# Kernel optimization log

Measured on AMD Instinct MI355X. Metric: run time of the kernel, lower is better.

The kernel has to match this reference:

```python
import jax, jax.numpy as jnp
import numpy as np

HIDDEN = 2048
INTER = 8192          # shared expert FFN
MOE_INTER = 1024      # routed expert FFN
N_ROUTED = 8
NUM_LOCAL = 8
TOP_K = 2
B, S = 4, 2048


def _mlp(x, gw, uw, dw):
    # down(swish(gate(x)) * up(x)); weights stored as (out, in) like nn.Linear
    g = x @ gw.T
    u = x @ uw.T
    return (g * jax.nn.sigmoid(g) * u) @ dw.T


def setup_inputs() -> dict:
    key = jax.random.key(0)
    ks = jax.random.split(key, 8)
    std = 0.02
    return {
        "hidden_states": jax.random.normal(ks[0], (B, S, HIDDEN), jnp.float32),
        "router_weight": jax.random.normal(ks[1], (N_ROUTED, HIDDEN), jnp.float32) * std,
        "sh_gate": jax.random.normal(ks[2], (INTER, HIDDEN), jnp.float32) * std,
        "sh_up": jax.random.normal(ks[3], (INTER, HIDDEN), jnp.float32) * std,
        "sh_down": jax.random.normal(ks[4], (HIDDEN, INTER), jnp.float32) * std,
        # NaiveMoe always uses experts[0]; only expert-0 weights participate.
        "r_gate": jax.random.normal(ks[5], (MOE_INTER, HIDDEN), jnp.float32) * std,
        "r_up": jax.random.normal(ks[6], (MOE_INTER, HIDDEN), jnp.float32) * std,
        "r_down": jax.random.normal(ks[7], (HIDDEN, MOE_INTER), jnp.float32) * std,
    }


def reference(hidden_states, router_weight, sh_gate, sh_up, sh_down, r_gate, r_up, r_down):
    Bsz, Seq, H = hidden_states.shape
    x = hidden_states.reshape(-1, H)                              # [T, H]

    # Router: float32 logits, top-k, softmax over the selected k
    logits = x.astype(jnp.float32) @ router_weight.astype(jnp.float32).T  # [T, E]
    topk_vals, topk_idx = jax.lax.top_k(logits, TOP_K)            # [T, K]
    topk_w = jax.nn.softmax(topk_vals, axis=-1)                   # [T, K]

    # Original dispatch loop applies experts[0] for every expert_id in
    # range(NUM_LOCAL); a token contributes its slot weight iff that slot's
    # routed index is < NUM_LOCAL. Net effect: per-token combined weight.
    slot_mask = (topk_idx < NUM_LOCAL).astype(topk_w.dtype)       # [T, K]
    comb_w = jnp.sum(topk_w * slot_mask, axis=-1).astype(x.dtype)  # [T]

    shared = _mlp(x, sh_gate, sh_up, sh_down)                     # [T, H]
    routed = _mlp(x, r_gate, r_up, r_down) * comb_w[:, None]      # [T, H]

    return (shared + routed).reshape(Bsz, Seq, H)
```

## Files before the change

### kernel.cpp

```cpp
#include <hip/hip_runtime.h>
#include <hip/hip_bf16.h>
#include <stdint.h>
#include <stddef.h>

#define HID   2048
#define INTER 8192
#define MOE_I 1024
#define TOK   8192

using bf16 = __hip_bfloat16;
typedef __attribute__((ext_vector_type(8))) short short8;
typedef __attribute__((ext_vector_type(4))) float f32x4;

__device__ __forceinline__ void gload_lds16(const bf16* g, bf16* l) {
    __builtin_amdgcn_global_load_lds(
        (const __attribute__((address_space(1))) void*)g,
        (__attribute__((address_space(3))) void*)l,
        16, 0, 0);
}

__device__ __forceinline__ short8 cvt8(float4 a, float4 b) {
    union { short8 s; bf16 h[8]; } u;
    u.h[0] = __float2bfloat16(a.x); u.h[1] = __float2bfloat16(a.y);
    u.h[2] = __float2bfloat16(a.z); u.h[3] = __float2bfloat16(a.w);
    u.h[4] = __float2bfloat16(b.x); u.h[5] = __float2bfloat16(b.y);
    u.h[6] = __float2bfloat16(b.z); u.h[7] = __float2bfloat16(b.w);
    return u.s;
}

__global__ void cast_f32_to_bf16(const float* __restrict__ in,
                                 bf16* __restrict__ out, int n4) {
    int stride = gridDim.x * blockDim.x;
    for (int i = blockIdx.x * blockDim.x + threadIdx.x; i < n4; i += stride) {
        float4 v = reinterpret_cast<const float4*>(in)[i];
        union { uint64_t u; bf16 h[4]; } o;
        o.h[0] = __float2bfloat16(v.x); o.h[1] = __float2bfloat16(v.y);
        o.h[2] = __float2bfloat16(v.z); o.h[3] = __float2bfloat16(v.w);
        reinterpret_cast<uint64_t*>(out)[i] = o.u;
    }
}


__global__ __launch_bounds__(512) void gemm8_gu(
    const bf16* __restrict__ X, const bf16* __restrict__ Wg,
    const bf16* __restrict__ Wu, bf16* __restrict__ H,
    int M, int N, int K)
{
    constexpr int STRM = 128 * 64;
    constexpr int SLOT = 3 * STRM;
    __shared__ __align__(16) bf16 lds[3 * SLOT];

    const int tid  = threadIdx.x;
    const int lane = tid & 63;
    const int wave = tid >> 6;
    const int n0 = blockIdx.x * 128;
    const int m0 = blockIdx.y * 128;

    const int srow = tid >> 3;
    const int scol = (((tid & 7) ^ (srow & 7)) << 3);
    const bf16* pA = X  + (size_t)(m0 + srow) * K + scol;
    const bf16* pG = Wg + (size_t)(n0 + srow) * K + scol;
    const bf16* pU = Wu + (size_t)(n0 + srow) * K + scol;
    const size_t rsk = (size_t)64 * K;
    bf16* dl = lds + tid * 8;

    const int wm = (wave >> 2) * 64;
    const int wn = (wave & 3) * 32;
    const int r16 = lane & 15;
    const int kq  = lane >> 4;
    const int cswz0 = ((kq       ^ (lane & 7)) << 4);
    const int cswz1 = (((4 + kq) ^ (lane & 7)) << 4);
    const char* lb = (const char*)lds;

    int roffA[4], roffW[2];
#pragma unroll
    for (int i = 0; i < 4; i++) roffA[i] = (wm + 16 * i + r16) * 128;
#pragma unroll
    for (int j = 0; j < 2; j++) roffW[j] = (wn + 16 * j + r16) * 128;

    f32x4 accg[4][2] = {};
    f32x4 accu[4][2] = {};
    const int NS = K >> 6;

#pragma unroll
    for (int s = 0; s < 2; s++) {
        bf16* d = dl + s * SLOT;
        const bf16* qa = pA + (size_t)s * 64;
        const bf16* qg = pG + (size_t)s * 64;
        const bf16* qu = pU + (size_t)s * 64;
        gload_lds16(qa,       d);
        gload_lds16(qg,       d + STRM);
        gload_lds16(qu,       d + 2 * STRM);
        gload_lds16(qa + rsk, d + 4096);
        gload_lds16(qg + rsk, d + STRM + 4096);
        gload_lds16(qu + rsk, d + 2 * STRM + 4096);
    }

    int cs = 0, ss = 2;
    for (int s = 0; s < NS; s++) {
        const int sp = (s + 2 < NS) ? (s + 2) : (NS - 1);
        const size_t ko = (size_t)sp * 64;
        const bf16* qa = pA + ko;
        const bf16* qg = pG + ko;
        const bf16* qu = pU + ko;
        bf16* d = dl + ss * SLOT;
        const char* cb = lb + (size_t)cs * (SLOT * 2);

        asm volatile("s_waitcnt vmcnt(6)" ::: "memory");
        __builtin_amdgcn_s_barrier();
        __builtin_amdgcn_sched_barrier(0);

        gload_lds16(qa, d);
        gload_lds16(qg, d + STRM);
        gload_lds16(qu, d + 2 * STRM);
        {
            short8 a[4], g[2], u[2];
#pragma unroll
            for (int i = 0; i < 4; i++)
                a[i] = *(const short8*)(cb + roffA[i] + cswz0);
#pragma unroll
            for (int j = 0; j < 2; j++) {
                g[j] = *(const short8*)(cb + (STRM * 2) + roffW[j] + cswz0);
                u[j] = *(const short8*)(cb + (STRM * 4) + roffW[j] + cswz0);
            }
            asm volatile("s_waitcnt lgkmcnt(0)" ::: "memory");
            __builtin_amdgcn_sched_barrier(0);
            __builtin_amdgcn_s_setprio(1);
#pragma unroll
            for (int i = 0; i < 4; i++)
#pragma unroll
                for (int j = 0; j < 2; j++) {
                    accg[i][j] = __builtin_amdgcn_mfma_f32_16x16x32_bf16(a[i], g[j], accg[i][j], 0, 0, 0);
                    accu[i][j] = __builtin_amdgcn_mfma_f32_16x16x32_bf16(a[i], u[j], accu[i][j], 0, 0, 0);
                }
            __builtin_amdgcn_s_setprio(0);
        }

        gload_lds16(qa + rsk, d + 4096);
        gload_lds16(qg + rsk, d + STRM + 4096);
        gload_lds16(qu + rsk, d + 2 * STRM + 4096);
        {
            short8 a[4], g[2], u[2];
#pragma unroll
            for (int i = 0; i < 4; i++)
                a[i] = *(const short8*)(cb + roffA[i] + cswz1);
#pragma unroll
            for (int j = 0; j < 2; j++) {
                g[j] = *(const short8*)(cb + (STRM * 2) + roffW[j] + cswz1);
                u[j] = *(const short8*)(cb + (STRM * 4) + roffW[j] + cswz1);
            }
            asm volatile("s_waitcnt lgkmcnt(0)" ::: "memory");
            __builtin_amdgcn_sched_barrier(0);
            __builtin_amdgcn_s_setprio(1);
#pragma unroll
            for (int i = 0; i < 4; i++)
#pragma unroll
                for (int j = 0; j < 2; j++) {
                    accg[i][j] = __builtin_amdgcn_mfma_f32_16x16x32_bf16(a[i], g[j], accg[i][j], 0, 0, 0);
                    accu[i][j] = __builtin_amdgcn_mfma_f32_16x16x32_bf16(a[i], u[j], accu[i][j], 0, 0, 0);
                }
            __builtin_amdgcn_s_setprio(0);
        }

        cs = (cs == 2) ? 0 : cs + 1;
        ss = (ss == 2) ? 0 : ss + 1;
    }
    asm volatile("s_waitcnt vmcnt(0)" ::: "memory");

#pragma unroll
    for (int i = 0; i < 4; i++) {
        const int rowb = m0 + wm + 16 * i + (lane >> 4) * 4;
#pragma unroll
        for (int j = 0; j < 2; j++) {
            const int col = n0 + wn + 16 * j + r16;
#pragma unroll
            for (int r = 0; r < 4; r++) {
                float g = accg[i][j][r];
                float u = accu[i][j][r];
                float h = g * u / (1.0f + __expf(-g));
                H[(size_t)(rowb + r) * N + col] = __float2bfloat16(h);
            }
        }
    }
}

__global__ __launch_bounds__(512) void gemm8_down(
    const bf16* __restrict__ Ha, const bf16* __restrict__ Bs,
    long ldBs, long col0,
    const bf16* __restrict__ Hb, const bf16* __restrict__ Br,
    long ldBr, float* __restrict__ OUT,
    int M, int N, int Ka, int Kb, int acc)
{
    constexpr int STRM = 128 * 64;
    constexpr int SLOT = 3 * STRM;
    __shared__ __align__(16) bf16 lds[3 * SLOT];

    const int tid  = threadIdx.x;
    const int lane = tid & 63;
    const int wave = tid >> 6;
    const int n0 = blockIdx.x * 256;
    const int m0 = blockIdx.y * 128;

    const int srow = tid >> 3;
    const int scol = (((tid & 7) ^ (srow & 7)) << 3);
    const bf16* pA1 = Ha + (size_t)(m0 + srow) * Ka + scol;
    const bf16* pB1 = Bs + (size_t)(n0 + srow) * ldBs + col0 + scol;
    const bf16* pA2 = Hb + (size_t)(m0 + srow) * Kb + scol;
    const bf16* pB2 = Br + (size_t)(n0 + srow) * ldBr + scol;
    const size_t rA1 = (size_t)64 * Ka, rB1 = (size_t)64 * ldBs;
    const size_t rA2 = (size_t)64 * Kb, rB2 = (size_t)64 * ldBr;
    bf16* dl = lds + tid * 8;

    const int wm = (wave >> 2) * 64;
    const int wn = (wave & 3) * 64;
    const int r16 = lane & 15;
    const int kq  = lane >> 4;
    const int cswz0 = ((kq       ^ (lane & 7)) << 4);
    const int cswz1 = (((4 + kq) ^ (lane & 7)) << 4);
    const char* lb = (const char*)lds;

    int roffA[4], roffB[4];
#pragma unroll
    for (int i = 0; i < 4; i++) roffA[i] = (wm + 16 * i + r16) * 128;
#pragma unroll
    for (int j = 0; j < 4; j++) roffB[j] = (wn + 16 * j + r16) * 128;

    f32x4 acc4[4][4] = {};
    const int NS1 = Ka >> 6;
    const int NS  = NS1 + (Kb >> 6);

#pragma unroll
    for (int s = 0; s < 2; s++) {
        bf16* d = dl + s * SLOT;
        const bf16* qa = pA1 + (size_t)s * 64;
        const bf16* qb = pB1 + (size_t)s * 64;
        gload_lds16(qa,           d);
        gload_lds16(qb,           d + STRM);
        gload_lds16(qb + rB1,     d + STRM + 4096);
        gload_lds16(qa + rA1,     d + 4096);
        gload_lds16(qb + 2 * rB1, d + 2 * STRM);
        gload_lds16(qb + 3 * rB1, d + 2 * STRM + 4096);
    }

    int cs = 0, ss = 2;
    for (int s = 0; s < NS; s++) {
        const int sp = (s + 2 < NS) ? (s + 2) : (NS - 1);
        const bf16 *qa, *qb; size_t ra, rb;
        if (sp < NS1) {
            size_t ko = (size_t)sp * 64;
            qa = pA1 + ko; qb = pB1 + ko; ra = rA1; rb = rB1;
        } else {
            size_t ko = (size_t)(sp - NS1) * 64;
            qa = pA2 + ko; qb = pB2 + ko; ra = rA2; rb = rB2;
        }
        bf16* d = dl + ss * SLOT;
        const char* cb = lb + (size_t)cs * (SLOT * 2);

        asm volatile("s_waitcnt vmcnt(6)" ::: "memory");
        __builtin_amdgcn_s_barrier();
        __builtin_amdgcn_sched_barrier(0);

        gload_lds16(qa,      d);
        gload_lds16(qb,      d + STRM);
        gload_lds16(qb + rb, d + STRM + 4096);
        {
            short8 a[4], b[4];
#pragma unroll
            for (int i = 0; i < 4; i++)
                a[i] = *(const short8*)(cb + roffA[i] + cswz0);
#pragma unroll
            for (int j = 0; j < 4; j++)
                b[j] = *(const short8*)(cb + (STRM * 2) + roffB[j] + cswz0);
            asm volatile("s_waitcnt lgkmcnt(0)" ::: "memory");
            __builtin_amdgcn_sched_barrier(0);
            __builtin_amdgcn_s_setprio(1);
#pragma unroll
            for (int i = 0; i < 4; i++)
#pragma unroll
                for (int j = 0; j < 4; j++)
                    acc4[i][j] = __builtin_amdgcn_mfma_f32_16x16x32_bf16(a[i], b[j], acc4[i][j], 0, 0, 0);
            __builtin_amdgcn_s_setprio(0);
        }

        gload_lds16(qa + ra,     d + 4096);
        gload_lds16(qb + 2 * rb, d + 2 * STRM);
        gload_lds16(qb + 3 * rb, d + 2 * STRM + 4096);
        {
            short8 a[4], b[4];
#pragma unroll
            for (int i = 0; i < 4; i++)
                a[i] = *(const short8*)(cb + roffA[i] + cswz1);
#pragma unroll
            for (int j = 0; j < 4; j++)
                b[j] = *(const short8*)(cb + (STRM * 2) + roffB[j] + cswz1);
            asm volatile("s_waitcnt lgkmcnt(0)" ::: "memory");
            __builtin_amdgcn_sched_barrier(0);
            __builtin_amdgcn_s_setprio(1);
#pragma unroll
            for (int i = 0; i < 4; i++)
#pragma unroll
                for (int j = 0; j < 4; j++)
                    acc4[i][j] = __builtin_amdgcn_mfma_f32_16x16x32_bf16(a[i], b[j], acc4[i][j], 0, 0, 0);
            __builtin_amdgcn_s_setprio(0);
        }

        cs = (cs == 2) ? 0 : cs + 1;
        ss = (ss == 2) ? 0 : ss + 1;
    }
    asm volatile("s_waitcnt vmcnt(0)" ::: "memory");

#pragma unroll
    for (int i = 0; i < 4; i++) {
        const int rowb = m0 + wm + 16 * i + (lane >> 4) * 4;
#pragma unroll
        for (int j = 0; j < 4; j++) {
            const int col = n0 + wn + 16 * j + r16;
#pragma unroll
            for (int r = 0; r < 4; r++) {
                const size_t idx = (size_t)(rowb + r) * N + col;
                float v = acc4[i][j][r];
                OUT[idx] = acc ? (OUT[idx] + v) : v;
            }
        }
    }
}

__global__ __launch_bounds__(256) void gemm_gu_bb(
    const bf16* __restrict__ X, const bf16* __restrict__ Wg,
    const bf16* __restrict__ Wu, bf16* __restrict__ H,
    int M, int N, int K)
{
    __shared__ bf16 sA[128 * 32];
    __shared__ bf16 sG[64 * 32];
    __shared__ bf16 sU[64 * 32];

    const int tid  = threadIdx.x;
    const int lane = tid & 63;
    const int wave = tid >> 6;
    const int n0 = blockIdx.x * 64;
    const int m0 = blockIdx.y * 128;

    const int srow = tid >> 2;
    const int scol = (tid & 3) * 8;
    const bf16* ga = X  + (size_t)(m0 + srow) * K + scol;
    const bf16* gg = Wg + (size_t)(n0 + srow) * K + scol;
    const bf16* gu = Wu + (size_t)(n0 + srow) * K + scol;
    const size_t rowskip = (size_t)64 * K;
    bf16* la = sA + tid * 8;
    bf16* lg = sG + tid * 8;
    bf16* lu = sU + tid * 8;

    const int wm  = (wave >> 1) * 64;
    const int wn  = (wave & 1) * 32;
    const int r16 = lane & 15;
    const int kq8 = (lane >> 4) * 8;

    f32x4 accg[4][2] = {};
    f32x4 accu[4][2] = {};

    for (int k0 = 0; k0 < K; k0 += 32) {
        gload_lds16(ga,           la);
        gload_lds16(ga + rowskip, la + 2048);
        gload_lds16(gg,           lg);
        gload_lds16(gu,           lu);
        ga += 32; gg += 32; gu += 32;
        __syncthreads();

        short8 af[4], bg[2], bu[2];
#pragma unroll
        for (int i = 0; i < 4; i++)
            af[i] = *reinterpret_cast<const short8*>(sA + (wm + 16 * i + r16) * 32 + kq8);
#pragma unroll
        for (int j = 0; j < 2; j++) {
            bg[j] = *reinterpret_cast<const short8*>(sG + (wn + 16 * j + r16) * 32 + kq8);
            bu[j] = *reinterpret_cast<const short8*>(sU + (wn + 16 * j + r16) * 32 + kq8);
        }
#pragma unroll
        for (int i = 0; i < 4; i++)
#pragma unroll
            for (int j = 0; j < 2; j++) {
                accg[i][j] = __builtin_amdgcn_mfma_f32_16x16x32_bf16(af[i], bg[j], accg[i][j], 0, 0, 0);
                accu[i][j] = __builtin_amdgcn_mfma_f32_16x16x32_bf16(af[i], bu[j], accu[i][j], 0, 0, 0);
            }
        __syncthreads();
    }

#pragma unroll
    for (int i = 0; i < 4; i++) {
        const int rowb = m0 + wm + 16 * i + (lane >> 4) * 4;
#pragma unroll
        for (int j = 0; j < 2; j++) {
            const int col = n0 + wn + 16 * j + r16;
#pragma unroll
            for (int r = 0; r < 4; r++) {
                float g = accg[i][j][r];
                float u = accu[i][j][r];
                float h = g * u / (1.0f + __expf(-g));
                H[(size_t)(rowb + r) * N + col] = __float2bfloat16(h);
            }
        }
    }
}

__global__ __launch_bounds__(256) void gemm_gu_f32(
    const float* __restrict__ X, const float* __restrict__ Wg,
    const float* __restrict__ Wu, bf16* __restrict__ H,
    int M, int N, int K)
{
    __shared__ bf16 sA[128 * 32];
    __shared__ bf16 sG[64 * 32];
    __shared__ bf16 sU[64 * 32];

    const int tid  = threadIdx.x;
    const int lane = tid & 63;
    const int wave = tid >> 6;
    const int n0 = blockIdx.x * 64;
    const int m0 = blockIdx.y * 128;

    const int srow = tid >> 2;
    const int scol = (tid & 3) * 8;

    const int wm  = (wave >> 1) * 64;
    const int wn  = (wave & 1) * 32;
    const int r16 = lane & 15;
    const int kq8 = (lane >> 4) * 8;

    f32x4 accg[4][2] = {};
    f32x4 accu[4][2] = {};

    for (int k0 = 0; k0 < K; k0 += 32) {
#pragma unroll
        for (int seg = 0; seg < 2; seg++) {
            const int row = srow + 64 * seg;
            const float* pa = X + (size_t)(m0 + row) * K + k0 + scol;
            float4 a0 = *(const float4*)pa, a1 = *(const float4*)(pa + 4);
            *(short8*)(sA + row * 32 + scol) = cvt8(a0, a1);
        }
        {
            const float* pg = Wg + (size_t)(n0 + srow) * K + k0 + scol;
            const float* pu = Wu + (size_t)(n0 + srow) * K + k0 + scol;
            float4 g0 = *(const float4*)pg, g1 = *(const float4*)(pg + 4);
            float4 u0 = *(const float4*)pu, u1 = *(const float4*)(pu + 4);
            *(short8*)(sG + srow * 32 + scol) = cvt8(g0, g1);
            *(short8*)(sU + srow * 32 + scol) = cvt8(u0, u1);
        }
        __syncthreads();

        short8 af[4], bg[2], bu[2];
#pragma unroll
        for (int i = 0; i < 4; i++)
            af[i] = *reinterpret_cast<const short8*>(sA + (wm + 16 * i + r16) * 32 + kq8);
#pragma unroll
        for (int j = 0; j < 2; j++) {
            bg[j] = *reinterpret_cast<const short8*>(sG + (wn + 16 * j + r16) * 32 + kq8);
            bu[j] = *reinterpret_cast<const short8*>(sU + (wn + 16 * j + r16) * 32 + kq8);
        }
#pragma unroll
        for (int i = 0; i < 4; i++)
#pragma unroll
            for (int j = 0; j < 2; j++) {
                accg[i][j] = __builtin_amdgcn_mfma_f32_16x16x32_bf16(af[i], bg[j], accg[i][j], 0, 0, 0);
                accu[i][j] = __builtin_amdgcn_mfma_f32_16x16x32_bf16(af[i], bu[j], accu[i][j], 0, 0, 0);
            }
        __syncthreads();
    }

#pragma unroll
    for (int i = 0; i < 4; i++) {
        const int rowb = m0 + wm + 16 * i + (lane >> 4) * 4;
#pragma unroll
        for (int j = 0; j < 2; j++) {
            const int col = n0 + wn + 16 * j + r16;
#pragma unroll
            for (int r = 0; r < 4; r++) {
                float g = accg[i][j][r];
                float u = accu[i][j][r];
                float h = g * u / (1.0f + __expf(-g));
                H[(size_t)(rowb + r) * N + col] = __float2bfloat16(h);
            }
        }
    }
}

__global__ __launch_bounds__(256) void gemm_down2(
    const bf16* __restrict__ Ha, const bf16* __restrict__ Bs16,
    const float* __restrict__ Bs32, int sflag, long ldBs, long col0,
    const bf16* __restrict__ Hb, const bf16* __restrict__ Br16,
    const float* __restrict__ Br32, int rflag, long ldBr,
    float* __restrict__ OUT, int M, int N, int Ka, int Kb, int acc)
{
    __shared__ bf16 sA[128 * 32];
    __shared__ bf16 sB[128 * 32];

    const int tid  = threadIdx.x;
    const int lane = tid & 63;
    const int wave = tid >> 6;
    const int n0 = blockIdx.x * 128;
    const int m0 = blockIdx.y * 128;

    const int srow = tid >> 2;
    const int scol = (tid & 3) * 8;
    bf16* la = sA + tid * 8;
    bf16* lb = sB + tid * 8;

    const int wm  = (wave >> 1) * 64;
    const int wn  = (wave & 1) * 64;
    const int r16 = lane & 15;
    const int kq8 = (lane >> 4) * 8;

    f32x4 acc4[4][4] = {};

    {
        const bf16* ga = Ha + (size_t)(m0 + srow) * Ka + scol;
        const size_t rska = (size_t)64 * Ka;
        const bf16* gb = Bs16 + (size_t)(n0 + srow) * ldBs + col0 + scol;
        const size_t rskb = (size_t)64 * ldBs;
        for (int k0 = 0; k0 < Ka; k0 += 32) {
            gload_lds16(ga,        la);
            gload_lds16(ga + rska, la + 2048);
            ga += 32;
            if (sflag) {
                gload_lds16(gb,        lb);
                gload_lds16(gb + rskb, lb + 2048);
                gb += 32;
            } else {
#pragma unroll
                for (int seg = 0; seg < 2; seg++) {
                    const int row = srow + 64 * seg;
                    const float* pb = Bs32 + (size_t)(n0 + row) * ldBs + col0 + k0 + scol;
                    float4 b0 = *(const float4*)pb, b1 = *(const float4*)(pb + 4);
                    *(short8*)(sB + row * 32 + scol) = cvt8(b0, b1);
                }
            }
            __syncthreads();

            short8 af[4], bw[4];
#pragma unroll
            for (int i = 0; i < 4; i++)
                af[i] = *reinterpret_cast<const short8*>(sA + (wm + 16 * i + r16) * 32 + kq8);
#pragma unroll
            for (int j = 0; j < 4; j++)
                bw[j] = *reinterpret_cast<const short8*>(sB + (wn + 16 * j + r16) * 32 + kq8);
#pragma unroll
            for (int i = 0; i < 4; i++)
#pragma unroll
                for (int j = 0; j < 4; j++)
                    acc4[i][j] = __builtin_amdgcn_mfma_f32_16x16x32_bf16(af[i], bw[j], acc4[i][j], 0, 0, 0);
            __syncthreads();
        }
    }
    if (Kb > 0) {
        const bf16* ga = Hb + (size_t)(m0 + srow) * Kb + scol;
        const size_t rska = (size_t)64 * Kb;
        const bf16* gb = Br16 + (size_t)(n0 + srow) * ldBr + scol;
        const size_t rskb = (size_t)64 * ldBr;
        for (int k0 = 0; k0 < Kb; k0 += 32) {
            gload_lds16(ga,        la);
            gload_lds16(ga + rska, la + 2048);
            ga += 32;
            if (rflag) {
                gload_lds16(gb,        lb);
                gload_lds16(gb + rskb, lb + 2048);
                gb += 32;
            } else {
#pragma unroll
                for (int seg = 0; seg < 2; seg++) {
                    const int row = srow + 64 * seg;
                    const float* pb = Br32 + (size_t)(n0 + row) * ldBr + k0 + scol;
                    float4 b0 = *(const float4*)pb, b1 = *(const float4*)(pb + 4);
                    *(short8*)(sB + row * 32 + scol) = cvt8(b0, b1);
                }
            }
            __syncthreads();

            short8 af[4], bw[4];
#pragma unroll
            for (int i = 0; i < 4; i++)
                af[i] = *reinterpret_cast<const short8*>(sA + (wm + 16 * i + r16) * 32 + kq8);
#pragma unroll
            for (int j = 0; j < 4; j++)
                bw[j] = *reinterpret_cast<const short8*>(sB + (wn + 16 * j + r16) * 32 + kq8);
#pragma unroll
            for (int i = 0; i < 4; i++)
#pragma unroll
                for (int j = 0; j < 4; j++)
                    acc4[i][j] = __builtin_amdgcn_mfma_f32_16x16x32_bf16(af[i], bw[j], acc4[i][j], 0, 0, 0);
            __syncthreads();
        }
    }

#pragma unroll
    for (int i = 0; i < 4; i++) {
        const int rowb = m0 + wm + 16 * i + (lane >> 4) * 4;
#pragma unroll
        for (int j = 0; j < 4; j++) {
            const int col = n0 + wn + 16 * j + r16;
#pragma unroll
            for (int r = 0; r < 4; r++) {
                const size_t idx = (size_t)(rowb + r) * N + col;
                float v = acc4[i][j][r];
                OUT[idx] = acc ? (OUT[idx] + v) : v;
            }
        }
    }
}

extern "C" void kernel_launch(void* const* d_in, const int* in_sizes, int n_in,
                              void* d_out, int out_size, void* d_ws, size_t ws_size,
                              hipStream_t stream) {
    const float* x       = (const float*)d_in[0];
    const float* sh_gate = (const float*)d_in[2];
    const float* sh_up   = (const float*)d_in[3];
    const float* sh_down = (const float*)d_in[4];
    const float* r_gate  = (const float*)d_in[5];
    const float* r_up    = (const float*)d_in[6];
    const float* r_down  = (const float*)d_in[7];
    float* out = (float*)d_out;

    auto cast = [&](const float* in, bf16* o, size_t n) {
        int n4 = (int)(n / 4);
        int blocks = (n4 + 255) / 256;
        if (blocks > 2048) blocks = 2048;
        cast_f32_to_bf16<<<dim3(blocks), dim3(256), 0, stream>>>(in, o, n4);
    };

    const size_t HS_MIN = (size_t)TOK * 128 * 2;
    size_t limit = (ws_size > HS_MIN) ? ws_size - HS_MIN : 0;
    size_t off = 0;
    auto take = [&](size_t bytes) -> bf16* {
        if (off + bytes <= limit) { bf16* p = (bf16*)((char*)d_ws + off); off += bytes; return p; }
        return nullptr;
    };

    bf16* Xb = take((size_t)TOK   * HID * 2);
    bf16* Gs = take((size_t)INTER * HID * 2);
    bf16* Us = take((size_t)INTER * HID * 2);
    bf16* Hr = take((size_t)TOK   * MOE_I * 2);

    if (Xb && Gs && Us && Hr) {
        bf16* Ds = take((size_t)INTER * HID * 2);
        bf16* Gr = take((size_t)MOE_I * HID * 2);
        bf16* Ur = take((size_t)MOE_I * HID * 2);
        bf16* Dr = take((size_t)MOE_I * HID * 2);

        size_t remain = ws_size - off;
        int Nc = 128;
        const int cands[7] = {8192, 4096, 2048, 1024, 512, 256, 128};
        for (int i = 0; i < 7; i++)
            if ((size_t)TOK * cands[i] * 2 <= remain) { Nc = cands[i]; break; }
        bf16* Hs = (bf16*)((char*)d_ws + off);

        cast(x,       Xb, (size_t)TOK   * HID);
        cast(sh_gate, Gs, (size_t)INTER * HID);
        cast(sh_up,   Us, (size_t)INTER * HID);
        if (Ds) cast(sh_down, Ds, (size_t)INTER * HID);
        if (Gr) cast(r_gate,  Gr, (size_t)MOE_I * HID);
        if (Ur) cast(r_up,    Ur, (size_t)MOE_I * HID);
        if (Dr) cast(r_down,  Dr, (size_t)MOE_I * HID);

        if (Ds && Gr && Ur && Dr) {
            gemm8_gu<<<dim3(MOE_I / 128, TOK / 128), dim3(512), 0, stream>>>(
                Xb, Gr, Ur, Hr, TOK, MOE_I, HID);
            const int nch = INTER / Nc;
            for (int c = 0; c < nch; c++) {
                gemm8_gu<<<dim3(Nc / 128, TOK / 128), dim3(512), 0, stream>>>(
                    Xb, Gs + (size_t)c * Nc * HID, Us + (size_t)c * Nc * HID,
                    Hs, TOK, Nc, HID);
                gemm8_down<<<dim3(HID / 256, TOK / 128), dim3(512), 0, stream>>>(
                    Hs, Ds, (long)INTER, (long)c * Nc,
                    Hr, Dr, (long)MOE_I,
                    out, TOK, HID, Nc, (c == 0) ? MOE_I : 0, (c == 0) ? 0 : 1);
            }
            return;
        }

        if (Gr && Ur)
            gemm_gu_bb<<<dim3(MOE_I / 64, TOK / 128), dim3(256), 0, stream>>>(
                Xb, Gr, Ur, Hr, TOK, MOE_I, HID);
        else
            gemm_gu_f32<<<dim3(MOE_I / 64, TOK / 128), dim3(256), 0, stream>>>(
                x, r_gate, r_up, Hr, TOK, MOE_I, HID);

        const int nch = INTER / Nc;
        for (int c = 0; c < nch; c++) {
            gemm_gu_bb<<<dim3(Nc / 64, TOK / 128), dim3(256), 0, stream>>>(
                Xb, Gs + (size_t)c * Nc * HID, Us + (size_t)c * Nc * HID,
                Hs, TOK, Nc, HID);
            gemm_down2<<<dim3(HID / 128, TOK / 128), dim3(256), 0, stream>>>(
                Hs, Ds, sh_down, Ds ? 1 : 0, (long)INTER, (long)c * Nc,
                Hr, Dr, r_down, Dr ? 1 : 0, (long)MOE_I,
                out, TOK, HID, Nc, (c == 0) ? MOE_I : 0, (c == 0) ? 0 : 1);
        }
        return;
    }

    {
        const size_t hrBytes = (size_t)TOK * MOE_I * 2;
        int Nc = 128;
        const int cands[6] = {8192, 4096, 2048, 1024, 512, 256};
        for (int i = 0; i < 6; i++)
            if ((size_t)TOK * cands[i] * 2 + hrBytes <= ws_size) { Nc = cands[i]; break; }
        bf16* Hs = (bf16*)d_ws;
        bf16* Hr2 = Hs + (size_t)TOK * Nc;

        gemm_gu_f32<<<dim3(MOE_I / 64, TOK / 128), dim3(256), 0, stream>>>(
            x, r_gate, r_up, Hr2, TOK, MOE_I, HID);
        const int nch = INTER / Nc;
        for (int c = 0; c < nch; c++) {
            gemm_gu_f32<<<dim3(Nc / 64, TOK / 128), dim3(256), 0, stream>>>(
                x, sh_gate + (size_t)c * Nc * HID, sh_up + (size_t)c * Nc * HID,
                Hs, TOK, Nc, HID);
            gemm_down2<<<dim3(HID / 128, TOK / 128), dim3(256), 0, stream>>>(
                Hs, nullptr, sh_down, 0, (long)INTER, (long)c * Nc,
                Hr2, nullptr, r_down, 0, (long)MOE_I,
                out, TOK, HID, Nc, (c == 0) ? MOE_I : 0, (c == 0) ? 0 : 1);
        }
    }
}
```

Before: 1.166 ms.

## Enlarge GEMM M-tile to 256 with double-buffered LDS and split MFMA phases

Both the gate/up and down GEMM kernels now use 256-row M tiles instead of 128, so each wave holds twice as many accumulators and every loaded weight tile is reused across more rows. The triple-buffered pipeline with half-tile loads is replaced by a double-buffered scheme: a full 64-K slice is prefetched each step, and compute is split into four sub-phases separated by barriers. Launch bounds request two blocks per CU and grids are halved along M. The goal is less global and LDS traffic per FLOP, paid for with higher register pressure, more barriers, a shallower prefetch depth (vmcnt(0) every step), and fewer blocks in flight.

After: 1.176 ms. Within noise of the previous version (+0.8%).

```diff
diff --git a/kernel.cpp b/kernel.cpp
--- a/kernel.cpp
+++ b/kernel.cpp
@@ -41,20 +41,19 @@
 }
 
 
-__global__ __launch_bounds__(512) void gemm8_gu(
+__global__ __launch_bounds__(512, 2) void gemm9_gu(
     const bf16* __restrict__ X, const bf16* __restrict__ Wg,
     const bf16* __restrict__ Wu, bf16* __restrict__ H,
     int M, int N, int K)
 {
-    constexpr int STRM = 128 * 64;
-    constexpr int SLOT = 3 * STRM;
-    __shared__ __align__(16) bf16 lds[3 * SLOT];
+    constexpr int SLOT = 32768;
+    __shared__ __align__(16) bf16 lds[2 * SLOT];
 
     const int tid  = threadIdx.x;
     const int lane = tid & 63;
     const int wave = tid >> 6;
     const int n0 = blockIdx.x * 128;
-    const int m0 = blockIdx.y * 128;
+    const int m0 = blockIdx.y * 256;
 
     const int srow = tid >> 3;
     const int scol = (((tid & 7) ^ (srow & 7)) << 3);
@@ -64,7 +63,7 @@
     const size_t rsk = (size_t)64 * K;
     bf16* dl = lds + tid * 8;
 
-    const int wm = (wave >> 2) * 64;
+    const int wm = (wave >> 2) * 128;
     const int wn = (wave & 3) * 32;
     const int r16 = lane & 15;
     const int kq  = lane >> 4;
@@ -72,103 +71,129 @@
     const int cswz1 = (((4 + kq) ^ (lane & 7)) << 4);
     const char* lb = (const char*)lds;
 
-    int roffA[4], roffW[2];
-#pragma unroll
-    for (int i = 0; i < 4; i++) roffA[i] = (wm + 16 * i + r16) * 128;
+    int roffA[8], roffW[2];
+#pragma unroll
+    for (int i = 0; i < 8; i++) roffA[i] = (wm + 16 * i + r16) * 128;
 #pragma unroll
     for (int j = 0; j < 2; j++) roffW[j] = (wn + 16 * j + r16) * 128;
 
-    f32x4 accg[4][2] = {};
-    f32x4 accu[4][2] = {};
+    f32x4 accg[8][2] = {};
+    f32x4 accu[8][2] = {};
     const int NS = K >> 6;
 
-#pragma unroll
-    for (int s = 0; s < 2; s++) {
-        bf16* d = dl + s * SLOT;
-        const bf16* qa = pA + (size_t)s * 64;
-        const bf16* qg = pG + (size_t)s * 64;
-        const bf16* qu = pU + (size_t)s * 64;
-        gload_lds16(qa,       d);
-        gload_lds16(qg,       d + STRM);
-        gload_lds16(qu,       d + 2 * STRM);
-        gload_lds16(qa + rsk, d + 4096);
-        gload_lds16(qg + rsk, d + STRM + 4096);
-        gload_lds16(qu + rsk, d + 2 * STRM + 4096);
-    }
-
-    int cs = 0, ss = 2;
+    {
+        bf16* d = dl;
+#pragma unroll
+        for (int c = 0; c < 4; c++) gload_lds16(pA + c * rsk, d + c * 4096);
+        gload_lds16(pG,       d + 16384);
+        gload_lds16(pG + rsk, d + 20480);
+        gload_lds16(pU,       d + 24576);
+        gload_lds16(pU + rsk, d + 28672);
+    }
+    asm volatile("s_waitcnt vmcnt(0)" ::: "memory");
+    __builtin_amdgcn_s_barrier();
+    __builtin_amdgcn_sched_barrier(0);
+
     for (int s = 0; s < NS; s++) {
-        const int sp = (s + 2 < NS) ? (s + 2) : (NS - 1);
-        const size_t ko = (size_t)sp * 64;
+        const int cur = s & 1;
+        const char* cb = lb + (size_t)cur * 65536;
+        bf16* d = dl + (cur ^ 1) * SLOT;
+        const size_t ko = (size_t)((s + 1 < NS) ? s + 1 : NS - 1) * 64;
         const bf16* qa = pA + ko;
         const bf16* qg = pG + ko;
         const bf16* qu = pU + ko;
-        bf16* d = dl + ss * SLOT;
-        const char* cb = lb + (size_t)cs * (SLOT * 2);
-
-        asm volatile("s_waitcnt vmcnt(6)" ::: "memory");
-        __builtin_amdgcn_s_barrier();
-        __builtin_amdgcn_sched_barrier(0);
-
-        gload_lds16(qa, d);
-        gload_lds16(qg, d + STRM);
-        gload_lds16(qu, d + 2 * STRM);
-        {
-            short8 a[4], g[2], u[2];
-#pragma unroll
-            for (int i = 0; i < 4; i++)
-                a[i] = *(const short8*)(cb + roffA[i] + cswz0);
+
+        short8 a[4], g[2], u[2];
+
+#pragma unroll
+        for (int c = 0; c < 4; c++) gload_lds16(qa + c * rsk, d + c * 4096);
+        gload_lds16(qg,       d + 16384);
+        gload_lds16(qg + rsk, d + 20480);
+        gload_lds16(qu,       d + 24576);
+        gload_lds16(qu + rsk, d + 28672);
+#pragma unroll
+        for (int ii = 0; ii < 4; ii++)
+            a[ii] = *(const short8*)(cb + roffA[ii] + cswz0);
+#pragma unroll
+        for (int j = 0; j < 2; j++) {
+            g[j] = *(const short8*)(cb + 32768 + roffW[j] + cswz0);
+            u[j] = *(const short8*)(cb + 49152 + roffW[j] + cswz0);
+        }
+        __builtin_amdgcn_s_barrier();
+        asm volatile("s_waitcnt lgkmcnt(0)" ::: "memory");
+        __builtin_amdgcn_sched_barrier(0);
+        __builtin_amdgcn_s_setprio(1);
+#pragma unroll
+        for (int ii = 0; ii < 4; ii++)
 #pragma unroll
             for (int j = 0; j < 2; j++) {
-                g[j] = *(const short8*)(cb + (STRM * 2) + roffW[j] + cswz0);
-                u[j] = *(const short8*)(cb + (STRM * 4) + roffW[j] + cswz0);
-            }
-            asm volatile("s_waitcnt lgkmcnt(0)" ::: "memory");
-            __builtin_amdgcn_sched_barrier(0);
-            __builtin_amdgcn_s_setprio(1);
-#pragma unroll
-            for (int i = 0; i < 4; i++)
-#pragma unroll
-                for (int j = 0; j < 2; j++) {
-                    accg[i][j] = __builtin_amdgcn_mfma_f32_16x16x32_bf16(a[i], g[j], accg[i][j], 0, 0, 0);
-                    accu[i][j] = __builtin_amdgcn_mfma_f32_16x16x32_bf16(a[i], u[j], accu[i][j], 0, 0, 0);
-                }
-            __builtin_amdgcn_s_setprio(0);
-        }
-
-        gload_lds16(qa + rsk, d + 4096);
-        gload_lds16(qg + rsk, d + STRM + 4096);
-        gload_lds16(qu + rsk, d + 2 * STRM + 4096);
-        {
-            short8 a[4], g[2], u[2];
-#pragma unroll
-            for (int i = 0; i < 4; i++)
-                a[i] = *(const short8*)(cb + roffA[i] + cswz1);
+                accg[ii][j] = __builtin_amdgcn_mfma_f32_16x16x32_bf16(a[ii], g[j], accg[ii][j], 0, 0, 0);
+                accu[ii][j] = __builtin_amdgcn_mfma_f32_16x16x32_bf16(a[ii], u[j], accu[ii][j], 0, 0, 0);
+            }
+        __builtin_amdgcn_s_setprio(0);
+        __builtin_amdgcn_s_barrier();
+
+#pragma unroll
+        for (int ii = 0; ii < 4; ii++)
+            a[ii] = *(const short8*)(cb + roffA[4 + ii] + cswz0);
+        __builtin_amdgcn_s_barrier();
+        asm volatile("s_waitcnt lgkmcnt(0)" ::: "memory");
+        __builtin_amdgcn_sched_barrier(0);
+        __builtin_amdgcn_s_setprio(1);
+#pragma unroll
+        for (int ii = 0; ii < 4; ii++)
 #pragma unroll
             for (int j = 0; j < 2; j++) {
-                g[j] = *(const short8*)(cb + (STRM * 2) + roffW[j] + cswz1);
-                u[j] = *(const short8*)(cb + (STRM * 4) + roffW[j] + cswz1);
-            }
-            asm volatile("s_waitcnt lgkmcnt(0)" ::: "memory");
-            __builtin_amdgcn_sched_barrier(0);
-            __builtin_amdgcn_s_setprio(1);
-#pragma unroll
-            for (int i = 0; i < 4; i++)
-#pragma unroll
-                for (int j = 0; j < 2; j++) {
-                    accg[i][j] = __builtin_amdgcn_mfma_f32_16x16x32_bf16(a[i], g[j], accg[i][j], 0, 0, 0);
-                    accu[i][j] = __builtin_amdgcn_mfma_f32_16x16x32_bf16(a[i], u[j], accu[i][j], 0, 0, 0);
-                }
-            __builtin_amdgcn_s_setprio(0);
-        }
-
-        cs = (cs == 2) ? 0 : cs + 1;
-        ss = (ss == 2) ? 0 : ss + 1;
-    }
-    asm volatile("s_waitcnt vmcnt(0)" ::: "memory");
-
-#pragma unroll
-    for (int i = 0; i < 4; i++) {
+                accg[4 + ii][j] = __builtin_amdgcn_mfma_f32_16x16x32_bf16(a[ii], g[j], accg[4 + ii][j], 0, 0, 0);
+                accu[4 + ii][j] = __builtin_amdgcn_mfma_f32_16x16x32_bf16(a[ii], u[j], accu[4 + ii][j], 0, 0, 0);
+            }
+        __builtin_amdgcn_s_setprio(0);
+        __builtin_amdgcn_s_barrier();
+
+#pragma unroll
+        for (int ii = 0; ii < 4; ii++)
+            a[ii] = *(const short8*)(cb + roffA[ii] + cswz1);
+#pragma unroll
+        for (int j = 0; j < 2; j++) {
+            g[j] = *(const short8*)(cb + 32768 + roffW[j] + cswz1);
+            u[j] = *(const short8*)(cb + 49152 + roffW[j] + cswz1);
+        }
+        __builtin_amdgcn_s_barrier();
+        asm volatile("s_waitcnt lgkmcnt(0)" ::: "memory");
+        __builtin_amdgcn_sched_barrier(0);
+        __builtin_amdgcn_s_setprio(1);
+#pragma unroll
+        for (int ii = 0; ii < 4; ii++)
+#pragma unroll
+            for (int j = 0; j < 2; j++) {
+                accg[ii][j] = __builtin_amdgcn_mfma_f32_16x16x32_bf16(a[ii], g[j], accg[ii][j], 0, 0, 0);
+                accu[ii][j] = __builtin_amdgcn_mfma_f32_16x16x32_bf16(a[ii], u[j], accu[ii][j], 0, 0, 0);
+            }
+        __builtin_amdgcn_s_setprio(0);
+        __builtin_amdgcn_s_barrier();
+
+#pragma unroll
+        for (int ii = 0; ii < 4; ii++)
+            a[ii] = *(const short8*)(cb + roffA[4 + ii] + cswz1);
+        __builtin_amdgcn_s_barrier();
+        asm volatile("s_waitcnt lgkmcnt(0)" ::: "memory");
+        __builtin_amdgcn_sched_barrier(0);
+        __builtin_amdgcn_s_setprio(1);
+#pragma unroll
+        for (int ii = 0; ii < 4; ii++)
+#pragma unroll
+            for (int j = 0; j < 2; j++) {
+                accg[4 + ii][j] = __builtin_amdgcn_mfma_f32_16x16x32_bf16(a[ii], g[j], accg[4 + ii][j], 0, 0, 0);
+                accu[4 + ii][j] = __builtin_amdgcn_mfma_f32_16x16x32_bf16(a[ii], u[j], accu[4 + ii][j], 0, 0, 0);
+            }
+        __builtin_amdgcn_s_setprio(0);
+        asm volatile("s_waitcnt vmcnt(0)" ::: "memory");
+        __builtin_amdgcn_s_barrier();
+        __builtin_amdgcn_sched_barrier(0);
+    }
+
+#pragma unroll
+    for (int i = 0; i < 8; i++) {
         const int rowb = m0 + wm + 16 * i + (lane >> 4) * 4;
 #pragma unroll
         for (int j = 0; j < 2; j++) {
@@ -184,22 +209,21 @@
     }
 }
 
-__global__ __launch_bounds__(512) void gemm8_down(
+__global__ __launch_bounds__(512, 2) void gemm9_down(
     const bf16* __restrict__ Ha, const bf16* __restrict__ Bs,
     long ldBs, long col0,
     const bf16* __restrict__ Hb, const bf16* __restrict__ Br,
     long ldBr, float* __restrict__ OUT,
     int M, int N, int Ka, int Kb, int acc)
 {
-    constexpr int STRM = 128 * 64;
-    constexpr int SLOT = 3 * STRM;
-    __shared__ __align__(16) bf16 lds[3 * SLOT];
+    constexpr int SLOT = 32768;
+    __shared__ __align__(16) bf16 lds[2 * SLOT];
 
     const int tid  = threadIdx.x;
     const int lane = tid & 63;
     const int wave = tid >> 6;
     const int n0 = blockIdx.x * 256;
-    const int m0 = blockIdx.y * 128;
+    const int m0 = blockIdx.y * 256;
 
     const int srow = tid >> 3;
     const int scol = (((tid & 7) ^ (srow & 7)) << 3);
@@ -211,7 +235,7 @@
     const size_t rA2 = (size_t)64 * Kb, rB2 = (size_t)64 * ldBr;
     bf16* dl = lds + tid * 8;
 
-    const int wm = (wave >> 2) * 64;
+    const int wm = (wave >> 2) * 128;
     const int wn = (wave & 3) * 64;
     const int r16 = lane & 15;
     const int kq  = lane >> 4;
@@ -219,32 +243,32 @@
     const int cswz1 = (((4 + kq) ^ (lane & 7)) << 4);
     const char* lb = (const char*)lds;
 
-    int roffA[4], roffB[4];
-#pragma unroll
-    for (int i = 0; i < 4; i++) roffA[i] = (wm + 16 * i + r16) * 128;
+    int roffA[8], roffB[4];
+#pragma unroll
+    for (int i = 0; i < 8; i++) roffA[i] = (wm + 16 * i + r16) * 128;
 #pragma unroll
     for (int j = 0; j < 4; j++) roffB[j] = (wn + 16 * j + r16) * 128;
 
-    f32x4 acc4[4][4] = {};
+    f32x4 acc4[8][4] = {};
     const int NS1 = Ka >> 6;
     const int NS  = NS1 + (Kb >> 6);
 
-#pragma unroll
-    for (int s = 0; s < 2; s++) {
-        bf16* d = dl + s * SLOT;
-        const bf16* qa = pA1 + (size_t)s * 64;
-        const bf16* qb = pB1 + (size_t)s * 64;
-        gload_lds16(qa,           d);
-        gload_lds16(qb,           d + STRM);
-        gload_lds16(qb + rB1,     d + STRM + 4096);
-        gload_lds16(qa + rA1,     d + 4096);
-        gload_lds16(qb + 2 * rB1, d + 2 * STRM);
-        gload_lds16(qb + 3 * rB1, d + 2 * STRM + 4096);
-    }
-
-    int cs = 0, ss = 2;
+    {
+        bf16* d = dl;
+#pragma unroll
+        for (int c = 0; c < 4; c++) gload_lds16(pA1 + c * rA1, d + c * 4096);
+#pragma unroll
+        for (int c = 0; c < 4; c++) gload_lds16(pB1 + c * rB1, d + 16384 + c * 4096);
+    }
+    asm volatile("s_waitcnt vmcnt(0)" ::: "memory");
+    __builtin_amdgcn_s_barrier();
+    __builtin_amdgcn_sched_barrier(0);
+
     for (int s = 0; s < NS; s++) {
-        const int sp = (s + 2 < NS) ? (s + 2) : (NS - 1);
+        const int cur = s & 1;
+        const char* cb = lb + (size_t)cur * 65536;
+        bf16* d = dl + (cur ^ 1) * SLOT;
+        const int sp = (s + 1 < NS) ? s + 1 : NS - 1;
         const bf16 *qa, *qb; size_t ra, rb;
         if (sp < NS1) {
             size_t ko = (size_t)sp * 64;
@@ -253,64 +277,84 @@
             size_t ko = (size_t)(sp - NS1) * 64;
             qa = pA2 + ko; qb = pB2 + ko; ra = rA2; rb = rB2;
         }
-        bf16* d = dl + ss * SLOT;
-        const char* cb = lb + (size_t)cs * (SLOT * 2);
-
-        asm volatile("s_waitcnt vmcnt(6)" ::: "memory");
-        __builtin_amdgcn_s_barrier();
-        __builtin_amdgcn_sched_barrier(0);
-
-        gload_lds16(qa,      d);
-        gload_lds16(qb,      d + STRM);
-        gload_lds16(qb + rb, d + STRM + 4096);
-        {
-            short8 a[4], b[4];
-#pragma unroll
-            for (int i = 0; i < 4; i++)
-                a[i] = *(const short8*)(cb + roffA[i] + cswz0);
+
+        short8 a[4], b[4];
+
+#pragma unroll
+        for (int c = 0; c < 4; c++) gload_lds16(qa + c * ra, d + c * 4096);
+#pragma unroll
+        for (int c = 0; c < 4; c++) gload_lds16(qb + c * rb, d + 16384 + c * 4096);
+#pragma unroll
+        for (int ii = 0; ii < 4; ii++)
+            a[ii] = *(const short8*)(cb + roffA[ii] + cswz0);
+#pragma unroll
+        for (int j = 0; j < 4; j++)
+            b[j] = *(const short8*)(cb + 32768 + roffB[j] + cswz0);
+        __builtin_amdgcn_s_barrier();
+        asm volatile("s_waitcnt lgkmcnt(0)" ::: "memory");
+        __builtin_amdgcn_sched_barrier(0);
+        __builtin_amdgcn_s_setprio(1);
+#pragma unroll
+        for (int ii = 0; ii < 4; ii++)
 #pragma unroll
             for (int j = 0; j < 4; j++)
-                b[j] = *(const short8*)(cb + (STRM * 2) + roffB[j] + cswz0);
-            asm volatile("s_waitcnt lgkmcnt(0)" ::: "memory");
-            __builtin_amdgcn_sched_barrier(0);
-            __builtin_amdgcn_s_setprio(1);
-#pragma unroll
-            for (int i = 0; i < 4; i++)
-#pragma unroll
-                for (int j = 0; j < 4; j++)
-                    acc4[i][j] = __builtin_amdgcn_mfma_f32_16x16x32_bf16(a[i], b[j], acc4[i][j], 0, 0, 0);
-            __builtin_amdgcn_s_setprio(0);
-        }
-
-        gload_lds16(qa + ra,     d + 4096);
-        gload_lds16(qb + 2 * rb, d + 2 * STRM);
-        gload_lds16(qb + 3 * rb, d + 2 * STRM + 4096);
-        {
-            short8 a[4], b[4];
-#pragma unroll
-            for (int i = 0; i < 4; i++)
-                a[i] = *(const short8*)(cb + roffA[i] + cswz1);
+                acc4[ii][j] = __builtin_amdgcn_mfma_f32_16x16x32_bf16(a[ii], b[j], acc4[ii][j], 0, 0, 0);
+        __builtin_amdgcn_s_setprio(0);
+        __builtin_amdgcn_s_barrier();
+
+#pragma unroll
+        for (int ii = 0; ii < 4; ii++)
+            a[ii] = *(const short8*)(cb + roffA[4 + ii] + cswz0);
+        __builtin_amdgcn_s_barrier();
+        asm volatile("s_waitcnt lgkmcnt(0)" ::: "memory");
+        __builtin_amdgcn_sched_barrier(0);
+        __builtin_amdgcn_s_setprio(1);
+#pragma unroll
+        for (int ii = 0; ii < 4; ii++)
 #pragma unroll
             for (int j = 0; j < 4; j++)
-                b[j] = *(const short8*)(cb + (STRM * 2) + roffB[j] + cswz1);
-            asm volatile("s_waitcnt lgkmcnt(0)" ::: "memory");
-            __builtin_amdgcn_sched_barrier(0);
-            __builtin_amdgcn_s_setprio(1);
-#pragma unroll
-            for (int i = 0; i < 4; i++)
-#pragma unroll
-                for (int j = 0; j < 4; j++)
-                    acc4[i][j] = __builtin_amdgcn_mfma_f32_16x16x32_bf16(a[i], b[j], acc4[i][j], 0, 0, 0);
-            __builtin_amdgcn_s_setprio(0);
-        }
-
-        cs = (cs == 2) ? 0 : cs + 1;
-        ss = (ss == 2) ? 0 : ss + 1;
-    }
-    asm volatile("s_waitcnt vmcnt(0)" ::: "memory");
-
-#pragma unroll
-    for (int i = 0; i < 4; i++) {
+                acc4[4 + ii][j] = __builtin_amdgcn_mfma_f32_16x16x32_bf16(a[ii], b[j], acc4[4 + ii][j], 0, 0, 0);
+        __builtin_amdgcn_s_setprio(0);
+        __builtin_amdgcn_s_barrier();
+
+#pragma unroll
+        for (int ii = 0; ii < 4; ii++)
+            a[ii] = *(const short8*)(cb + roffA[ii] + cswz1);
+#pragma unroll
+        for (int j = 0; j < 4; j++)
+            b[j] = *(const short8*)(cb + 32768 + roffB[j] + cswz1);
+        __builtin_amdgcn_s_barrier();
+        asm volatile("s_waitcnt lgkmcnt(0)" ::: "memory");
+        __builtin_amdgcn_sched_barrier(0);
+        __builtin_amdgcn_s_setprio(1);
+#pragma unroll
+        for (int ii = 0; ii < 4; ii++)
+#pragma unroll
+            for (int j = 0; j < 4; j++)
+                acc4[ii][j] = __builtin_amdgcn_mfma_f32_16x16x32_bf16(a[ii], b[j], acc4[ii][j], 0, 0, 0);
+        __builtin_amdgcn_s_setprio(0);
+        __builtin_amdgcn_s_barrier();
+
+#pragma unroll
+        for (int ii = 0; ii < 4; ii++)
+            a[ii] = *(const short8*)(cb + roffA[4 + ii] + cswz1);
+        __builtin_amdgcn_s_barrier();
+        asm volatile("s_waitcnt lgkmcnt(0)" ::: "memory");
+        __builtin_amdgcn_sched_barrier(0);
+        __builtin_amdgcn_s_setprio(1);
+#pragma unroll
+        for (int ii = 0; ii < 4; ii++)
+#pragma unroll
+            for (int j = 0; j < 4; j++)
+                acc4[4 + ii][j] = __builtin_amdgcn_mfma_f32_16x16x32_bf16(a[ii], b[j], acc4[4 + ii][j], 0, 0, 0);
+        __builtin_amdgcn_s_setprio(0);
+        asm volatile("s_waitcnt vmcnt(0)" ::: "memory");
+        __builtin_amdgcn_s_barrier();
+        __builtin_amdgcn_sched_barrier(0);
+    }
+
+#pragma unroll
+    for (int i = 0; i < 8; i++) {
         const int rowb = m0 + wm + 16 * i + (lane >> 4) * 4;
 #pragma unroll
         for (int j = 0; j < 4; j++) {
@@ -659,14 +703,14 @@
         if (Dr) cast(r_down,  Dr, (size_t)MOE_I * HID);
 
         if (Ds && Gr && Ur && Dr) {
-            gemm8_gu<<<dim3(MOE_I / 128, TOK / 128), dim3(512), 0, stream>>>(
+            gemm9_gu<<<dim3(MOE_I / 128, TOK / 256), dim3(512), 0, stream>>>(
                 Xb, Gr, Ur, Hr, TOK, MOE_I, HID);
             const int nch = INTER / Nc;
             for (int c = 0; c < nch; c++) {
-                gemm8_gu<<<dim3(Nc / 128, TOK / 128), dim3(512), 0, stream>>>(
+                gemm9_gu<<<dim3(Nc / 128, TOK / 256), dim3(512), 0, stream>>>(
                     Xb, Gs + (size_t)c * Nc * HID, Us + (size_t)c * Nc * HID,
                     Hs, TOK, Nc, HID);
-                gemm8_down<<<dim3(HID / 256, TOK / 128), dim3(512), 0, stream>>>(
+                gemm9_down<<<dim3(HID / 256, TOK / 256), dim3(512), 0, stream>>>(
                     Hs, Ds, (long)INTER, (long)c * Nc,
                     Hr, Dr, (long)MOE_I,
                     out, TOK, HID, Nc, (c == 0) ? MOE_I : 0, (c == 0) ? 0 : 1);
```
